# Kernel tuning notes

Measured on AMD Instinct MI355X. Metric: run time of the kernel, lower is better.

## Reference

```python
import jax, jax.numpy as jnp
import numpy as np

N_NODES = 100000
N_EDGES = 1200000
IN_DIM, HID_DIM, OUT_DIM = 64, 64, 32


def setup_inputs() -> dict:
    key = jax.random.key(0)
    k1, k2, k3, k4, k5, k6 = jax.random.split(key, 6)
    x = jax.random.normal(k1, (N_NODES, IN_DIM), dtype=jnp.float32)
    edge_index = jax.random.randint(k2, (2, N_EDGES), 0, N_NODES, dtype=jnp.int64)
    # Glorot-style init for GCN linear weights
    W1 = jax.random.normal(k3, (IN_DIM, HID_DIM), dtype=jnp.float32) / np.sqrt(IN_DIM)
    b1 = jnp.zeros((HID_DIM,), dtype=jnp.float32)
    W2 = jax.random.normal(k4, (HID_DIM, OUT_DIM), dtype=jnp.float32) / np.sqrt(HID_DIM)
    b2 = jnp.zeros((OUT_DIM,), dtype=jnp.float32)
    return {"x": x, "edge_index": edge_index, "W1": W1, "b1": b1, "W2": W2, "b2": b2}


def _gcn_conv(x, W, b, src, dst, norm, n_nodes):
    # linear transform first (PyG GCNConv): [N, out]
    h = x @ W
    # gather messages along edges (incl. self-loops), scale by sym norm
    msg = h[src] * norm[:, None]            # [E+N, out]
    out = jax.ops.segment_sum(msg, dst, num_segments=n_nodes)
    return out + b


def reference(x, edge_index, W1, b1, W2, b2):
    n_nodes = x.shape[0]
    # add self-loops (PyG GCNConv default)
    loop = jnp.arange(n_nodes, dtype=edge_index.dtype)
    src = jnp.concatenate([edge_index[0], loop])
    dst = jnp.concatenate([edge_index[1], loop])
    # symmetric normalization: deg^{-1/2}[src] * deg^{-1/2}[dst]
    deg = jax.ops.segment_sum(jnp.ones_like(dst, dtype=x.dtype), dst, num_segments=n_nodes)
    deg_isqrt = jax.lax.rsqrt(deg)          # deg >= 1 due to self-loops
    norm = deg_isqrt[src] * deg_isqrt[dst]
    h = _gcn_conv(x, W1, b1, src, dst, norm, n_nodes)
    h = jax.nn.relu(h)
    out = _gcn_conv(h, W2, b2, src, dst, norm, n_nodes)
    return out
```

## Files before the change

### kernel.cpp

```cpp
#include <hip/hip_runtime.h>
#include <hip/hip_fp16.h>
#include <type_traits>

#define NBUCK 512

typedef _Float16 half8 __attribute__((ext_vector_type(8)));
typedef float floatx4 __attribute__((ext_vector_type(4)));

__device__ inline void unpack8(const float4& raw, float* f) {
    const __half2* p = (const __half2*)&raw;
#pragma unroll
    for (int i = 0; i < 4; ++i) {
        float2 t = __half22float2(p[i]);
        f[2 * i] = t.x;
        f[2 * i + 1] = t.y;
    }
}


__global__ void bucket_hist_kernel(const int* __restrict__ dst, int* __restrict__ bucketCnt,
                                   int E, int R) {
    __shared__ int h[NBUCK];
    int tid = threadIdx.x;
    for (int i = tid; i < NBUCK; i += blockDim.x) h[i] = 0;
    __syncthreads();
    for (int i = blockIdx.x * blockDim.x + tid; i < E; i += gridDim.x * blockDim.x)
        atomicAdd(&h[dst[i] / R], 1);
    __syncthreads();
    for (int i = tid; i < NBUCK; i += blockDim.x)
        if (h[i]) atomicAdd(&bucketCnt[i], h[i]);
}


__global__ void bucket_scan_kernel(const int* __restrict__ bucketCnt, int* __restrict__ bucketBase,
                                   int* __restrict__ bucketCursor) {
    __shared__ int lds[NBUCK];
    int tid = threadIdx.x;
    int v = bucketCnt[tid];
    lds[tid] = v;
    __syncthreads();
    for (int off = 1; off < NBUCK; off <<= 1) {
        int x = (tid >= off) ? lds[tid - off] : 0;
        __syncthreads();
        lds[tid] += x;
        __syncthreads();
    }
    int excl = lds[tid] - v;
    bucketBase[tid] = excl;
    bucketCursor[tid] = excl;
    if (tid == NBUCK - 1) bucketBase[NBUCK] = lds[tid];
}


__global__ __launch_bounds__(1024) void partition_kernel(const int* __restrict__ src,
                                                         const int* __restrict__ dst,
                                                         int* __restrict__ bucketCursor,
                                                         unsigned long long* __restrict__ pairs,
                                                         int E, int R) {
    __shared__ int h[NBUCK];
    __shared__ int base[NBUCK];
    __shared__ int lcur[NBUCK];
    const int CH = 16384;
    int start = blockIdx.x * CH;
    int count = E - start;
    if (count > CH) count = CH;
    int tid = threadIdx.x;
    if (tid < NBUCK) h[tid] = 0;
    __syncthreads();
    for (int i = tid; i < count; i += 1024)
        atomicAdd(&h[dst[start + i] / R], 1);
    __syncthreads();
    if (tid < NBUCK) {
        base[tid] = h[tid] ? atomicAdd(&bucketCursor[tid], h[tid]) : 0;
        lcur[tid] = 0;
    }
    __syncthreads();
    for (int i = tid; i < count; i += 1024) {
        int d = dst[start + i];
        int s = src[start + i];
        int b = d / R;
        int r = atomicAdd(&lcur[b], 1);
        pairs[base[b] + r] = ((unsigned long long)(unsigned)s << 32) | (unsigned)d;
    }
}


__global__ void bucket_csr_kernel(const unsigned long long* __restrict__ pairs,
                                  const int* __restrict__ bucketBase, int* __restrict__ counts,
                                  int* __restrict__ offs, float* __restrict__ dinv,
                                  int* __restrict__ ssrc, int N, int R) {
    __shared__ int h[256];
    __shared__ int loffs[256];
    __shared__ int cur[256];
    int b = blockIdx.x, tid = threadIdx.x;
    int nodeBase = b * R;
    int beg = bucketBase[b], end = bucketBase[b + 1];
    h[tid] = 0;
    __syncthreads();
    for (int i = beg + tid; i < end; i += 256) {
        int d = (int)(pairs[i] & 0xffffffffull);
        atomicAdd(&h[d - nodeBase], 1);
    }
    __syncthreads();
    int v = h[tid];
    loffs[tid] = v;
    __syncthreads();
    for (int off = 1; off < 256; off <<= 1) {
        int x = (tid >= off) ? loffs[tid - off] : 0;
        __syncthreads();
        loffs[tid] += x;
        __syncthreads();
    }
    int excl = loffs[tid] - v;
    cur[tid] = excl;
    int node = nodeBase + tid;
    if (tid < R && node < N) {
        counts[node] = v;
        offs[node] = beg + excl;
        dinv[node] = rsqrtf((float)v + 1.0f);
    }
    __syncthreads();
    for (int i = beg + tid; i < end; i += 256) {
        unsigned long long p = pairs[i];
        int d = (int)(p & 0xffffffffull);
        int s = (int)(p >> 32);
        int r = atomicAdd(&cur[d - nodeBase], 1);
        ssrc[beg + r] = s;
    }
}


template <int OUTD, typename TIN>
__global__ void gemm_mfma_kernel(const TIN* __restrict__ X, const float* __restrict__ W,
                                 __half* __restrict__ H, int M, int ntiles) {
    constexpr int NC = OUTD / 16;
    const int lane = threadIdx.x & 63;
    const int wid  = threadIdx.x >> 6;
    const int q    = lane >> 4;
    const int m    = lane & 15;

    half8 bfrag[2][NC];
#pragma unroll
    for (int s = 0; s < 2; ++s)
#pragma unroll
        for (int c = 0; c < NC; ++c)
#pragma unroll
            for (int j = 0; j < 8; ++j)
                bfrag[s][c][j] = (_Float16)W[(s * 32 + q * 8 + j) * OUTD + c * 16 + m];

    for (int tile = blockIdx.x * 4 + wid; tile < ntiles; tile += gridDim.x * 4) {
        int rowBase = tile * 16;
        int rowA = rowBase + m;
        if (rowA > M - 1) rowA = M - 1;

        half8 afrag[2];
        if constexpr (std::is_same<TIN, float>::value) {
            const float4* Xr = (const float4*)(X + (size_t)rowA * 64);
#pragma unroll
            for (int s = 0; s < 2; ++s) {
                float4 v0 = Xr[s * 8 + q * 2 + 0];
                float4 v1 = Xr[s * 8 + q * 2 + 1];
                afrag[s][0] = (_Float16)v0.x;
                afrag[s][1] = (_Float16)v0.y;
                afrag[s][2] = (_Float16)v0.z;
                afrag[s][3] = (_Float16)v0.w;
                afrag[s][4] = (_Float16)v1.x;
                afrag[s][5] = (_Float16)v1.y;
                afrag[s][6] = (_Float16)v1.z;
                afrag[s][7] = (_Float16)v1.w;
            }
        } else {
            const half8* Xr = (const half8*)(X + (size_t)rowA * 64);
#pragma unroll
            for (int s = 0; s < 2; ++s)
                afrag[s] = Xr[s * 4 + q];
        }

        floatx4 acc[NC];
#pragma unroll
        for (int c = 0; c < NC; ++c) acc[c] = (floatx4){0.f, 0.f, 0.f, 0.f};
#pragma unroll
        for (int s = 0; s < 2; ++s)
#pragma unroll
            for (int c = 0; c < NC; ++c)
                acc[c] = __builtin_amdgcn_mfma_f32_16x16x32_f16(afrag[s], bfrag[s][c], acc[c],
                                                                0, 0, 0);

#pragma unroll
        for (int r = 0; r < 4; ++r) {
            int row = rowBase + q * 4 + r;
            if (row < M) {
#pragma unroll
                for (int c = 0; c < NC; ++c)
                    H[(size_t)row * OUTD + c * 16 + m] = __float2half(acc[c][r]);
            }
        }
    }
}


__global__ __launch_bounds__(256) void agg64_kernel(
    const float4* __restrict__ hrow4, const int* __restrict__ ssrc,
    const int* __restrict__ offs, const int* __restrict__ counts,
    const float* __restrict__ dinv, const float* __restrict__ b1,
    float4* __restrict__ out4, int N) {
    int tid  = threadIdx.x;
    int lane = tid & 63;
    int l    = tid & 7;
    int gb   = lane & 56;
    int node = blockIdx.x * 32 + (tid >> 3);
    if (node >= N) return;
    int beg = offs[node], cnt = counts[node];
    float a[8];
#pragma unroll
    for (int j = 0; j < 8; ++j) a[j] = 0.f;
    for (int base = 0; base < cnt; base += 8) {
        int p = base + l;
        int idx = 0;
        float dv = 0.0f;
        if (p < cnt) {
            idx = ssrc[beg + p];
            dv  = dinv[idx];
        }
#pragma unroll
        for (int j = 0; j < 8; ++j) {
            int   s  = __shfl(idx, gb | j, 64);
            float nv = __shfl(dv, gb | j, 64);
            float4 raw = hrow4[(size_t)s * 8 + l];
            float f[8];
            unpack8(raw, f);
#pragma unroll
            for (int d = 0; d < 8; ++d) a[d] = fmaf(f[d], nv, a[d]);
        }
    }
    float dd = dinv[node];
    float4 sraw = hrow4[(size_t)node * 8 + l];
    float sf[8];
    unpack8(sraw, sf);
    __half2 pk[4];
#pragma unroll
    for (int i = 0; i < 4; ++i) {
        float rx = fmaxf(dd * (a[2 * i] + sf[2 * i] * dd) + b1[8 * l + 2 * i], 0.0f);
        float ry = fmaxf(dd * (a[2 * i + 1] + sf[2 * i + 1] * dd) + b1[8 * l + 2 * i + 1], 0.0f);
        pk[i] = __floats2half2_rn(rx, ry);
    }
    out4[(size_t)node * 8 + l] = *(const float4*)pk;
}


__global__ __launch_bounds__(256) void agg32_kernel(
    const float4* __restrict__ hrow4, const int* __restrict__ ssrc,
    const int* __restrict__ offs, const int* __restrict__ counts,
    const float* __restrict__ dinv, const float* __restrict__ b2,
    float4* __restrict__ out4, int N) {
    int tid  = threadIdx.x;
    int lane = tid & 63;
    int l    = tid & 3;
    int gb   = lane & 60;
    int node = blockIdx.x * 64 + (tid >> 2);
    if (node >= N) return;
    int beg = offs[node], cnt = counts[node];
    float a[8];
#pragma unroll
    for (int j = 0; j < 8; ++j) a[j] = 0.f;
    for (int base = 0; base < cnt; base += 4) {
        int p = base + l;
        int idx = 0;
        float dv = 0.0f;
        if (p < cnt) {
            idx = ssrc[beg + p];
            dv  = dinv[idx];
        }
#pragma unroll
        for (int j = 0; j < 4; ++j) {
            int   s  = __shfl(idx, gb | j, 64);
            float nv = __shfl(dv, gb | j, 64);
            float4 raw = hrow4[(size_t)s * 4 + l];
            float f[8];
            unpack8(raw, f);
#pragma unroll
            for (int d = 0; d < 8; ++d) a[d] = fmaf(f[d], nv, a[d]);
        }
    }
    float dd = dinv[node];
    float4 sraw = hrow4[(size_t)node * 4 + l];
    float sf[8];
    unpack8(sraw, sf);
    float r[8];
#pragma unroll
    for (int j = 0; j < 8; ++j)
        r[j] = dd * (a[j] + sf[j] * dd) + b2[8 * l + j];
    out4[(size_t)node * 8 + 2 * l + 0] = make_float4(r[0], r[1], r[2], r[3]);
    out4[(size_t)node * 8 + 2 * l + 1] = make_float4(r[4], r[5], r[6], r[7]);
}


extern "C" void kernel_launch(void* const* d_in, const int* in_sizes, int n_in,
                              void* d_out, int out_size, void* d_ws, size_t ws_size,
                              hipStream_t stream) {
    const float* x  = (const float*)d_in[0];
    const int*   ei = (const int*)d_in[1];
    const float* W1 = (const float*)d_in[2];
    const float* b1 = (const float*)d_in[3];
    const float* W2 = (const float*)d_in[4];
    const float* b2 = (const float*)d_in[5];
    float* out = (float*)d_out;

    const int N = in_sizes[0] / 64;
    const int E = in_sizes[1] / 2;
    const int* src = ei;
    const int* dst = ei + E;

    const int Npad = (N + 1023) & ~1023;
    const int R    = (N + NBUCK - 1) / NBUCK;

    unsigned long long* pairs = (unsigned long long*)d_ws;
    int*   ssrc   = (int*)(pairs + E);
    int*   counts = ssrc + E;
    int*   offs   = counts + Npad;
    float* dinv   = (float*)(offs + Npad);
    int*   bucketCnt    = (int*)(dinv + Npad);
    int*   bucketBase   = bucketCnt + NBUCK;
    int*   bucketCursor = bucketBase + NBUCK + 1;
    size_t hoff = (size_t)(bucketCursor + NBUCK + 1 - (int*)d_ws);
    hoff = (hoff + 3) & ~(size_t)3;
    __half* h    = (__half*)((int*)d_ws + hoff);
    __half* out1 = h + (size_t)N * 64;
    __half* h2   = h;

    const int T = 256;

    hipMemsetAsync(bucketCnt, 0, NBUCK * sizeof(int), stream);
    bucket_hist_kernel<<<512, T, 0, stream>>>(dst, bucketCnt, E, R);
    bucket_scan_kernel<<<1, NBUCK, 0, stream>>>(bucketCnt, bucketBase, bucketCursor);
    partition_kernel<<<(E + 16383) / 16384, 1024, 0, stream>>>(src, dst, bucketCursor, pairs, E, R);
    bucket_csr_kernel<<<NBUCK, T, 0, stream>>>(pairs, bucketBase, counts, offs, dinv, ssrc, N, R);

    const int ntiles = (N + 15) / 16;

    gemm_mfma_kernel<64, float><<<782, T, 0, stream>>>(x, W1, h, N, ntiles);
    agg64_kernel<<<(N + 31) / 32, T, 0, stream>>>((const float4*)h, ssrc, offs, counts, dinv, b1,
                                                  (float4*)out1, N);

    gemm_mfma_kernel<32, __half><<<782, T, 0, stream>>>(out1, W2, h2, N, ntiles);
    agg32_kernel<<<(N + 63) / 64, T, 0, stream>>>((const float4*)h2, ssrc, offs, counts, dinv, b2,
                                                  (float4*)out, N);
}
```

Measured before the change: 220.1 us.

## Fuse histogram with first GEMM and use deterministic per-block scatter offsets

```diff
diff --git a/kernel.cpp b/kernel.cpp
--- a/kernel.cpp
+++ b/kernel.cpp
@@ -3,6 +3,7 @@
 #include <type_traits>
 
 #define NBUCK 512
+#define CH    2048
 
 typedef _Float16 half8 __attribute__((ext_vector_type(8)));
 typedef float floatx4 __attribute__((ext_vector_type(4)));
@@ -18,88 +19,165 @@
 }
 
 
-__global__ void bucket_hist_kernel(const int* __restrict__ dst, int* __restrict__ bucketCnt,
-                                   int E, int R) {
-    __shared__ int h[NBUCK];
-    int tid = threadIdx.x;
-    for (int i = tid; i < NBUCK; i += blockDim.x) h[i] = 0;
-    __syncthreads();
-    for (int i = blockIdx.x * blockDim.x + tid; i < E; i += gridDim.x * blockDim.x)
-        atomicAdd(&h[dst[i] / R], 1);
-    __syncthreads();
-    for (int i = tid; i < NBUCK; i += blockDim.x)
-        if (h[i]) atomicAdd(&bucketCnt[i], h[i]);
-}
-
-
-__global__ void bucket_scan_kernel(const int* __restrict__ bucketCnt, int* __restrict__ bucketBase,
-                                   int* __restrict__ bucketCursor) {
+__device__ inline void gemm64_f32_body(const float* __restrict__ X, const float* __restrict__ W,
+                                       __half* __restrict__ H, int M, int ntiles, int vblk,
+                                       int GB) {
+    constexpr int NC = 4;
+    const int lane = threadIdx.x & 63;
+    const int wid  = threadIdx.x >> 6;
+    const int q    = lane >> 4;
+    const int m    = lane & 15;
+
+    half8 bfrag[2][NC];
+#pragma unroll
+    for (int s = 0; s < 2; ++s)
+#pragma unroll
+        for (int c = 0; c < NC; ++c)
+#pragma unroll
+            for (int j = 0; j < 8; ++j)
+                bfrag[s][c][j] = (_Float16)W[(s * 32 + q * 8 + j) * 64 + c * 16 + m];
+
+    for (int tile = vblk * 4 + wid; tile < ntiles; tile += GB * 4) {
+        int rowBase = tile * 16;
+        int rowA = rowBase + m;
+        if (rowA > M - 1) rowA = M - 1;
+
+        half8 afrag[2];
+        const float4* Xr = (const float4*)(X + (size_t)rowA * 64);
+#pragma unroll
+        for (int s = 0; s < 2; ++s) {
+            float4 v0 = Xr[s * 8 + q * 2 + 0];
+            float4 v1 = Xr[s * 8 + q * 2 + 1];
+            afrag[s][0] = (_Float16)v0.x;
+            afrag[s][1] = (_Float16)v0.y;
+            afrag[s][2] = (_Float16)v0.z;
+            afrag[s][3] = (_Float16)v0.w;
+            afrag[s][4] = (_Float16)v1.x;
+            afrag[s][5] = (_Float16)v1.y;
+            afrag[s][6] = (_Float16)v1.z;
+            afrag[s][7] = (_Float16)v1.w;
+        }
+
+        floatx4 acc[NC];
+#pragma unroll
+        for (int c = 0; c < NC; ++c) acc[c] = (floatx4){0.f, 0.f, 0.f, 0.f};
+#pragma unroll
+        for (int s = 0; s < 2; ++s)
+#pragma unroll
+            for (int c = 0; c < NC; ++c)
+                acc[c] = __builtin_amdgcn_mfma_f32_16x16x32_f16(afrag[s], bfrag[s][c], acc[c],
+                                                                0, 0, 0);
+
+#pragma unroll
+        for (int r = 0; r < 4; ++r) {
+            int row = rowBase + q * 4 + r;
+            if (row < M) {
+#pragma unroll
+                for (int c = 0; c < NC; ++c)
+                    H[(size_t)row * 64 + c * 16 + m] = __float2half(acc[c][r]);
+            }
+        }
+    }
+}
+
+
+__global__ __launch_bounds__(256) void hist_gemm1_kernel(
+    const int* __restrict__ dst, int* __restrict__ blockHist,
+    const float* __restrict__ X, const float* __restrict__ W1, __half* __restrict__ H,
+    int M, int ntiles, int E, int R, int HB, int GB) {
+    int blk = blockIdx.x;
+    if (blk < HB) {
+        __shared__ int h[NBUCK];
+        int tid = threadIdx.x;
+        for (int i = tid; i < NBUCK; i += 256) h[i] = 0;
+        __syncthreads();
+        int start = blk * CH;
+        int count = E - start;
+        if (count > CH) count = CH;
+        for (int i = tid; i < count; i += 256) atomicAdd(&h[dst[start + i] / R], 1);
+        __syncthreads();
+        for (int i = tid; i < NBUCK; i += 256) blockHist[(size_t)blk * NBUCK + i] = h[i];
+    } else {
+        gemm64_f32_body(X, W1, H, M, ntiles, blk - HB, GB);
+    }
+}
+
+
+__global__ __launch_bounds__(NBUCK) void scan_bases_kernel(const int* __restrict__ blockHist,
+                                                           int* __restrict__ baseTbl,
+                                                           int* __restrict__ bucketStart, int HB) {
     __shared__ int lds[NBUCK];
-    int tid = threadIdx.x;
-    int v = bucketCnt[tid];
-    lds[tid] = v;
+    int b = threadIdx.x;
+    int running = 0;
+    int k = 0;
+    for (; k + 8 <= HB; k += 8) {
+        int v[8];
+#pragma unroll
+        for (int u = 0; u < 8; ++u) v[u] = blockHist[(size_t)(k + u) * NBUCK + b];
+#pragma unroll
+        for (int u = 0; u < 8; ++u) {
+            baseTbl[(size_t)(k + u) * NBUCK + b] = running;
+            running += v[u];
+        }
+    }
+    for (; k < HB; ++k) {
+        int v = blockHist[(size_t)k * NBUCK + b];
+        baseTbl[(size_t)k * NBUCK + b] = running;
+        running += v;
+    }
+    lds[b] = running;
     __syncthreads();
     for (int off = 1; off < NBUCK; off <<= 1) {
-        int x = (tid >= off) ? lds[tid - off] : 0;
-        __syncthreads();
-        lds[tid] += x;
-        __syncthreads();
-    }
-    int excl = lds[tid] - v;
-    bucketBase[tid] = excl;
-    bucketCursor[tid] = excl;
-    if (tid == NBUCK - 1) bucketBase[NBUCK] = lds[tid];
-}
-
-
-__global__ __launch_bounds__(1024) void partition_kernel(const int* __restrict__ src,
-                                                         const int* __restrict__ dst,
-                                                         int* __restrict__ bucketCursor,
-                                                         unsigned long long* __restrict__ pairs,
-                                                         int E, int R) {
-    __shared__ int h[NBUCK];
-    __shared__ int base[NBUCK];
+        int x = (b >= off) ? lds[b - off] : 0;
+        __syncthreads();
+        lds[b] += x;
+        __syncthreads();
+    }
+    bucketStart[b] = lds[b] - running;
+    if (b == NBUCK - 1) bucketStart[NBUCK] = lds[b];
+}
+
+
+__global__ __launch_bounds__(256) void scatter_kernel(
+    const int* __restrict__ src, const int* __restrict__ dst, const int* __restrict__ baseTbl,
+    const int* __restrict__ bucketStart, unsigned long long* __restrict__ pairs, int E, int R) {
     __shared__ int lcur[NBUCK];
-    const int CH = 16384;
-    int start = blockIdx.x * CH;
+    int blk = blockIdx.x, tid = threadIdx.x;
+    for (int i = tid; i < NBUCK; i += 256)
+        lcur[i] = bucketStart[i] + baseTbl[(size_t)blk * NBUCK + i];
+    __syncthreads();
+    int start = blk * CH;
     int count = E - start;
     if (count > CH) count = CH;
-    int tid = threadIdx.x;
-    if (tid < NBUCK) h[tid] = 0;
-    __syncthreads();
-    for (int i = tid; i < count; i += 1024)
-        atomicAdd(&h[dst[start + i] / R], 1);
-    __syncthreads();
-    if (tid < NBUCK) {
-        base[tid] = h[tid] ? atomicAdd(&bucketCursor[tid], h[tid]) : 0;
-        lcur[tid] = 0;
-    }
-    __syncthreads();
-    for (int i = tid; i < count; i += 1024) {
+    for (int i = tid; i < count; i += 256) {
         int d = dst[start + i];
         int s = src[start + i];
         int b = d / R;
         int r = atomicAdd(&lcur[b], 1);
-        pairs[base[b] + r] = ((unsigned long long)(unsigned)s << 32) | (unsigned)d;
-    }
-}
-
-
-__global__ void bucket_csr_kernel(const unsigned long long* __restrict__ pairs,
-                                  const int* __restrict__ bucketBase, int* __restrict__ counts,
-                                  int* __restrict__ offs, float* __restrict__ dinv,
-                                  int* __restrict__ ssrc, int N, int R) {
+        pairs[r] = ((unsigned long long)(unsigned)s << 32) | (unsigned)d;
+    }
+}
+
+
+__global__ __launch_bounds__(256) void bucket_csr_kernel(
+    const unsigned long long* __restrict__ pairs, const int* __restrict__ bucketStart,
+    int* __restrict__ counts, int* __restrict__ offs, float* __restrict__ dinv,
+    int* __restrict__ ssrc, int N, int R) {
+    __shared__ unsigned long long stage[3072];
     __shared__ int h[256];
     __shared__ int loffs[256];
     __shared__ int cur[256];
     int b = blockIdx.x, tid = threadIdx.x;
     int nodeBase = b * R;
-    int beg = bucketBase[b], end = bucketBase[b + 1];
+    int beg = bucketStart[b], end = bucketStart[b + 1];
+    int len = end - beg;
+    int sl = len < 3072 ? len : 3072;
+    for (int i = tid; i < sl; i += 256) stage[i] = pairs[beg + i];
     h[tid] = 0;
     __syncthreads();
-    for (int i = beg + tid; i < end; i += 256) {
-        int d = (int)(pairs[i] & 0xffffffffull);
-        atomicAdd(&h[d - nodeBase], 1);
+    for (int i = tid; i < len; i += 256) {
+        unsigned long long p = (i < 3072) ? stage[i] : pairs[beg + i];
+        atomicAdd(&h[(int)(p & 0xffffffffull) - nodeBase], 1);
     }
     __syncthreads();
     int v = h[tid];
@@ -120,20 +198,21 @@
         dinv[node] = rsqrtf((float)v + 1.0f);
     }
     __syncthreads();
-    for (int i = beg + tid; i < end; i += 256) {
-        unsigned long long p = pairs[i];
-        int d = (int)(p & 0xffffffffull);
+    for (int i = tid; i < len; i += 256) {
+        unsigned long long p = (i < 3072) ? stage[i] : pairs[beg + i];
+        int d = (int)(p & 0xffffffffull) - nodeBase;
         int s = (int)(p >> 32);
-        int r = atomicAdd(&cur[d - nodeBase], 1);
+        int r = atomicAdd(&cur[d], 1);
         ssrc[beg + r] = s;
     }
 }
 
 
-template <int OUTD, typename TIN>
-__global__ void gemm_mfma_kernel(const TIN* __restrict__ X, const float* __restrict__ W,
-                                 __half* __restrict__ H, int M, int ntiles) {
-    constexpr int NC = OUTD / 16;
+__global__ __launch_bounds__(256) void gemm2_mfma_kernel(const __half* __restrict__ X,
+                                                         const float* __restrict__ W,
+                                                         __half* __restrict__ H, int M,
+                                                         int ntiles) {
+    constexpr int NC = 2;
     const int lane = threadIdx.x & 63;
     const int wid  = threadIdx.x >> 6;
     const int q    = lane >> 4;
@@ -146,35 +225,17 @@
         for (int c = 0; c < NC; ++c)
 #pragma unroll
             for (int j = 0; j < 8; ++j)
-                bfrag[s][c][j] = (_Float16)W[(s * 32 + q * 8 + j) * OUTD + c * 16 + m];
+                bfrag[s][c][j] = (_Float16)W[(s * 32 + q * 8 + j) * 32 + c * 16 + m];
 
     for (int tile = blockIdx.x * 4 + wid; tile < ntiles; tile += gridDim.x * 4) {
         int rowBase = tile * 16;
         int rowA = rowBase + m;
         if (rowA > M - 1) rowA = M - 1;
 
+        const half8* Xr = (const half8*)(X + (size_t)rowA * 64);
         half8 afrag[2];
-        if constexpr (std::is_same<TIN, float>::value) {
-            const float4* Xr = (const float4*)(X + (size_t)rowA * 64);
-#pragma unroll
-            for (int s = 0; s < 2; ++s) {
-                float4 v0 = Xr[s * 8 + q * 2 + 0];
-                float4 v1 = Xr[s * 8 + q * 2 + 1];
-                afrag[s][0] = (_Float16)v0.x;
-                afrag[s][1] = (_Float16)v0.y;
-                afrag[s][2] = (_Float16)v0.z;
-                afrag[s][3] = (_Float16)v0.w;
-                afrag[s][4] = (_Float16)v1.x;
-                afrag[s][5] = (_Float16)v1.y;
-                afrag[s][6] = (_Float16)v1.z;
-                afrag[s][7] = (_Float16)v1.w;
-            }
-        } else {
-            const half8* Xr = (const half8*)(X + (size_t)rowA * 64);
-#pragma unroll
-            for (int s = 0; s < 2; ++s)
-                afrag[s] = Xr[s * 4 + q];
-        }
+#pragma unroll
+        for (int s = 0; s < 2; ++s) afrag[s] = Xr[s * 4 + q];
 
         floatx4 acc[NC];
 #pragma unroll
@@ -192,7 +253,7 @@
             if (row < M) {
 #pragma unroll
                 for (int c = 0; c < NC; ++c)
-                    H[(size_t)row * OUTD + c * 16 + m] = __float2half(acc[c][r]);
+                    H[(size_t)row * 32 + c * 16 + m] = __float2half(acc[c][r]);
             }
         }
     }
@@ -313,36 +374,34 @@
 
     const int Npad = (N + 1023) & ~1023;
     const int R    = (N + NBUCK - 1) / NBUCK;
+    const int HB   = (E + CH - 1) / CH;
+    const int GB   = 782;
 
     unsigned long long* pairs = (unsigned long long*)d_ws;
-    int*   ssrc   = (int*)(pairs + E);
-    int*   counts = ssrc + E;
-    int*   offs   = counts + Npad;
-    float* dinv   = (float*)(offs + Npad);
-    int*   bucketCnt    = (int*)(dinv + Npad);
-    int*   bucketBase   = bucketCnt + NBUCK;
-    int*   bucketCursor = bucketBase + NBUCK + 1;
-    size_t hoff = (size_t)(bucketCursor + NBUCK + 1 - (int*)d_ws);
+    int*   ssrc        = (int*)(pairs + E);
+    int*   counts      = ssrc + E;
+    int*   offs        = counts + Npad;
+    float* dinv        = (float*)(offs + Npad);
+    int*   bucketStart = (int*)(dinv + Npad);
+    int*   blockHist   = bucketStart + NBUCK + 2;
+    int*   baseTbl     = blockHist + (size_t)HB * NBUCK;
+    size_t hoff = (size_t)(baseTbl + (size_t)HB * NBUCK - (int*)d_ws);
     hoff = (hoff + 3) & ~(size_t)3;
     __half* h    = (__half*)((int*)d_ws + hoff);
     __half* out1 = h + (size_t)N * 64;
     __half* h2   = h;
 
-    const int T = 256;
-
-    hipMemsetAsync(bucketCnt, 0, NBUCK * sizeof(int), stream);
-    bucket_hist_kernel<<<512, T, 0, stream>>>(dst, bucketCnt, E, R);
-    bucket_scan_kernel<<<1, NBUCK, 0, stream>>>(bucketCnt, bucketBase, bucketCursor);
-    partition_kernel<<<(E + 16383) / 16384, 1024, 0, stream>>>(src, dst, bucketCursor, pairs, E, R);
-    bucket_csr_kernel<<<NBUCK, T, 0, stream>>>(pairs, bucketBase, counts, offs, dinv, ssrc, N, R);
-
     const int ntiles = (N + 15) / 16;
 
-    gemm_mfma_kernel<64, float><<<782, T, 0, stream>>>(x, W1, h, N, ntiles);
-    agg64_kernel<<<(N + 31) / 32, T, 0, stream>>>((const float4*)h, ssrc, offs, counts, dinv, b1,
-                                                  (float4*)out1, N);
-
-    gemm_mfma_kernel<32, __half><<<782, T, 0, stream>>>(out1, W2, h2, N, ntiles);
-    agg32_kernel<<<(N + 63) / 64, T, 0, stream>>>((const float4*)h2, ssrc, offs, counts, dinv, b2,
-                                                  (float4*)out, N);
-}
+    hist_gemm1_kernel<<<HB + GB, 256, 0, stream>>>(dst, blockHist, x, W1, h, N, ntiles,
+                                                   E, R, HB, GB);
+    scan_bases_kernel<<<1, NBUCK, 0, stream>>>(blockHist, baseTbl, bucketStart, HB);
+    scatter_kernel<<<HB, 256, 0, stream>>>(src, dst, baseTbl, bucketStart, pairs, E, R);
+    bucket_csr_kernel<<<NBUCK, 256, 0, stream>>>(pairs, bucketStart, counts, offs, dinv, ssrc,
+                                                 N, R);
+    agg64_kernel<<<(N + 31) / 32, 256, 0, stream>>>((const float4*)h, ssrc, offs, counts, dinv,
+                                                    b1, (float4*)out1, N);
+    gemm2_mfma_kernel<<<782, 256, 0, stream>>>(out1, W2, h2, N, ntiles);
+    agg32_kernel<<<(N + 63) / 64, 256, 0, stream>>>((const float4*)h2, ssrc, offs, counts, dinv,
+                                                    b2, (float4*)out, N);
+}
```

Result: slower. 227.3 us (+3.3%).

## Fuse histogram with layer-1 GEMM, use fixed-capacity buckets, fold W2 GEMV into aggregation

Applied to the files above, without the earlier changes.

```diff
diff --git a/kernel.cpp b/kernel.cpp
--- a/kernel.cpp
+++ b/kernel.cpp
@@ -1,8 +1,10 @@
 #include <hip/hip_runtime.h>
 #include <hip/hip_fp16.h>
-#include <type_traits>
 
 #define NBUCK 512
+#define CH    4096
+#define CAP   4096
+#define VTOT  1024
 
 typedef _Float16 half8 __attribute__((ext_vector_type(8)));
 typedef float floatx4 __attribute__((ext_vector_type(4)));
@@ -18,97 +20,130 @@
 }
 
 
-__global__ void bucket_hist_kernel(const int* __restrict__ dst, int* __restrict__ bucketCnt,
-                                   int E, int R) {
-    __shared__ int h[NBUCK];
-    int tid = threadIdx.x;
-    for (int i = tid; i < NBUCK; i += blockDim.x) h[i] = 0;
-    __syncthreads();
-    for (int i = blockIdx.x * blockDim.x + tid; i < E; i += gridDim.x * blockDim.x)
-        atomicAdd(&h[dst[i] / R], 1);
-    __syncthreads();
-    for (int i = tid; i < NBUCK; i += blockDim.x)
-        if (h[i]) atomicAdd(&bucketCnt[i], h[i]);
-}
-
-
-__global__ void bucket_scan_kernel(const int* __restrict__ bucketCnt, int* __restrict__ bucketBase,
-                                   int* __restrict__ bucketCursor) {
-    __shared__ int lds[NBUCK];
-    int tid = threadIdx.x;
-    int v = bucketCnt[tid];
-    lds[tid] = v;
-    __syncthreads();
-    for (int off = 1; off < NBUCK; off <<= 1) {
-        int x = (tid >= off) ? lds[tid - off] : 0;
+__global__ __launch_bounds__(256) void k_phaseA(
+    const int* __restrict__ dst, int* __restrict__ baseTbl, int* __restrict__ cursor,
+    const float* __restrict__ X, const float* __restrict__ W1, __half* __restrict__ H,
+    int M, int ntiles, int E, int R, int HB) {
+    int blk = blockIdx.x;
+    if (blk < HB) {
+        __shared__ int h[NBUCK];
+        int tid = threadIdx.x;
+        for (int i = tid; i < NBUCK; i += 256) h[i] = 0;
         __syncthreads();
-        lds[tid] += x;
+        int start = blk * CH;
+        int count = E - start;
+        if (count > CH) count = CH;
+        for (int i = tid; i < count; i += 256) atomicAdd(&h[dst[start + i] / R], 1);
         __syncthreads();
-    }
-    int excl = lds[tid] - v;
-    bucketBase[tid] = excl;
-    bucketCursor[tid] = excl;
-    if (tid == NBUCK - 1) bucketBase[NBUCK] = lds[tid];
-}
-
-
-__global__ __launch_bounds__(1024) void partition_kernel(const int* __restrict__ src,
-                                                         const int* __restrict__ dst,
-                                                         int* __restrict__ bucketCursor,
-                                                         unsigned long long* __restrict__ pairs,
-                                                         int E, int R) {
-    __shared__ int h[NBUCK];
-    __shared__ int base[NBUCK];
+        for (int i = tid; i < NBUCK; i += 256) {
+            int c = h[i];
+            int base = c ? atomicAdd(&cursor[i], c) : 0;
+            baseTbl[(size_t)blk * NBUCK + i] = base;
+        }
+    } else {
+        const int GB = VTOT - HB;
+        const int vblk = blk - HB;
+        const int lane = threadIdx.x & 63;
+        const int wid  = threadIdx.x >> 6;
+        const int q    = lane >> 4;
+        const int m    = lane & 15;
+
+        half8 bfrag[2][4];
+#pragma unroll
+        for (int s = 0; s < 2; ++s)
+#pragma unroll
+            for (int c = 0; c < 4; ++c)
+#pragma unroll
+                for (int j = 0; j < 8; ++j)
+                    bfrag[s][c][j] = (_Float16)W1[(s * 32 + q * 8 + j) * 64 + c * 16 + m];
+
+        for (int tile = vblk * 4 + wid; tile < ntiles; tile += GB * 4) {
+            int rowBase = tile * 16;
+            int rowA = rowBase + m;
+            if (rowA > M - 1) rowA = M - 1;
+            const float4* Xr = (const float4*)(X + (size_t)rowA * 64);
+            half8 afrag[2];
+#pragma unroll
+            for (int s = 0; s < 2; ++s) {
+                float4 v0 = Xr[s * 8 + q * 2 + 0];
+                float4 v1 = Xr[s * 8 + q * 2 + 1];
+                afrag[s][0] = (_Float16)v0.x; afrag[s][1] = (_Float16)v0.y;
+                afrag[s][2] = (_Float16)v0.z; afrag[s][3] = (_Float16)v0.w;
+                afrag[s][4] = (_Float16)v1.x; afrag[s][5] = (_Float16)v1.y;
+                afrag[s][6] = (_Float16)v1.z; afrag[s][7] = (_Float16)v1.w;
+            }
+            floatx4 acc[4];
+#pragma unroll
+            for (int c = 0; c < 4; ++c) acc[c] = (floatx4){0.f, 0.f, 0.f, 0.f};
+#pragma unroll
+            for (int s = 0; s < 2; ++s)
+#pragma unroll
+                for (int c = 0; c < 4; ++c)
+                    acc[c] = __builtin_amdgcn_mfma_f32_16x16x32_f16(afrag[s], bfrag[s][c],
+                                                                    acc[c], 0, 0, 0);
+#pragma unroll
+            for (int r = 0; r < 4; ++r) {
+                int row = rowBase + q * 4 + r;
+                if (row < M) {
+#pragma unroll
+                    for (int c = 0; c < 4; ++c)
+                        H[(size_t)row * 64 + c * 16 + m] = __float2half(acc[c][r]);
+                }
+            }
+        }
+    }
+}
+
+
+__global__ __launch_bounds__(256) void k_scatter(
+    const int* __restrict__ src, const int* __restrict__ dst, const int* __restrict__ baseTbl,
+    unsigned long long* __restrict__ pairs, int E, int R) {
     __shared__ int lcur[NBUCK];
-    const int CH = 16384;
-    int start = blockIdx.x * CH;
+    int blk = blockIdx.x, tid = threadIdx.x;
+    for (int i = tid; i < NBUCK; i += 256)
+        lcur[i] = i * CAP + baseTbl[(size_t)blk * NBUCK + i];
+    __syncthreads();
+    int start = blk * CH;
     int count = E - start;
     if (count > CH) count = CH;
-    int tid = threadIdx.x;
-    if (tid < NBUCK) h[tid] = 0;
-    __syncthreads();
-    for (int i = tid; i < count; i += 1024)
-        atomicAdd(&h[dst[start + i] / R], 1);
-    __syncthreads();
-    if (tid < NBUCK) {
-        base[tid] = h[tid] ? atomicAdd(&bucketCursor[tid], h[tid]) : 0;
-        lcur[tid] = 0;
-    }
-    __syncthreads();
-    for (int i = tid; i < count; i += 1024) {
+    for (int i = tid; i < count; i += 256) {
         int d = dst[start + i];
         int s = src[start + i];
         int b = d / R;
         int r = atomicAdd(&lcur[b], 1);
-        pairs[base[b] + r] = ((unsigned long long)(unsigned)s << 32) | (unsigned)d;
-    }
-}
-
-
-__global__ void bucket_csr_kernel(const unsigned long long* __restrict__ pairs,
-                                  const int* __restrict__ bucketBase, int* __restrict__ counts,
-                                  int* __restrict__ offs, float* __restrict__ dinv,
-                                  int* __restrict__ ssrc, int N, int R) {
+        pairs[r] = ((unsigned long long)(unsigned)s << 32) | (unsigned)d;
+    }
+}
+
+
+__global__ __launch_bounds__(256) void k_csr(
+    const unsigned long long* __restrict__ pairs, const int* __restrict__ cursor,
+    int* __restrict__ counts, int* __restrict__ offs, float* __restrict__ dinv,
+    int* __restrict__ ssrc, int N, int R) {
+    __shared__ unsigned long long stage[3072];
     __shared__ int h[256];
     __shared__ int loffs[256];
     __shared__ int cur[256];
     int b = blockIdx.x, tid = threadIdx.x;
     int nodeBase = b * R;
-    int beg = bucketBase[b], end = bucketBase[b + 1];
+    int beg = b * CAP;
+    int len = cursor[b];
+    int sl = len < 3072 ? len : 3072;
+    for (int i = tid; i < sl; i += 256) stage[i] = pairs[beg + i];
     h[tid] = 0;
     __syncthreads();
-    for (int i = beg + tid; i < end; i += 256) {
-        int d = (int)(pairs[i] & 0xffffffffull);
-        atomicAdd(&h[d - nodeBase], 1);
+    for (int i = tid; i < len; i += 256) {
+        unsigned long long pr = (i < 3072) ? stage[i] : pairs[beg + i];
+        atomicAdd(&h[(int)(pr & 0xffffffffull) - nodeBase], 1);
     }
     __syncthreads();
     int v = h[tid];
     loffs[tid] = v;
     __syncthreads();
     for (int off = 1; off < 256; off <<= 1) {
-        int x = (tid >= off) ? loffs[tid - off] : 0;
+        int xv = (tid >= off) ? loffs[tid - off] : 0;
         __syncthreads();
-        loffs[tid] += x;
+        loffs[tid] += xv;
         __syncthreads();
     }
     int excl = loffs[tid] - v;
@@ -120,90 +155,21 @@
         dinv[node] = rsqrtf((float)v + 1.0f);
     }
     __syncthreads();
-    for (int i = beg + tid; i < end; i += 256) {
-        unsigned long long p = pairs[i];
-        int d = (int)(p & 0xffffffffull);
-        int s = (int)(p >> 32);
-        int r = atomicAdd(&cur[d - nodeBase], 1);
+    for (int i = tid; i < len; i += 256) {
+        unsigned long long pr = (i < 3072) ? stage[i] : pairs[beg + i];
+        int d = (int)(pr & 0xffffffffull) - nodeBase;
+        int s = (int)(pr >> 32);
+        int r = atomicAdd(&cur[d], 1);
         ssrc[beg + r] = s;
     }
 }
 
 
-template <int OUTD, typename TIN>
-__global__ void gemm_mfma_kernel(const TIN* __restrict__ X, const float* __restrict__ W,
-                                 __half* __restrict__ H, int M, int ntiles) {
-    constexpr int NC = OUTD / 16;
-    const int lane = threadIdx.x & 63;
-    const int wid  = threadIdx.x >> 6;
-    const int q    = lane >> 4;
-    const int m    = lane & 15;
-
-    half8 bfrag[2][NC];
-#pragma unroll
-    for (int s = 0; s < 2; ++s)
-#pragma unroll
-        for (int c = 0; c < NC; ++c)
-#pragma unroll
-            for (int j = 0; j < 8; ++j)
-                bfrag[s][c][j] = (_Float16)W[(s * 32 + q * 8 + j) * OUTD + c * 16 + m];
-
-    for (int tile = blockIdx.x * 4 + wid; tile < ntiles; tile += gridDim.x * 4) {
-        int rowBase = tile * 16;
-        int rowA = rowBase + m;
-        if (rowA > M - 1) rowA = M - 1;
-
-        half8 afrag[2];
-        if constexpr (std::is_same<TIN, float>::value) {
-            const float4* Xr = (const float4*)(X + (size_t)rowA * 64);
-#pragma unroll
-            for (int s = 0; s < 2; ++s) {
-                float4 v0 = Xr[s * 8 + q * 2 + 0];
-                float4 v1 = Xr[s * 8 + q * 2 + 1];
-                afrag[s][0] = (_Float16)v0.x;
-                afrag[s][1] = (_Float16)v0.y;
-                afrag[s][2] = (_Float16)v0.z;
-                afrag[s][3] = (_Float16)v0.w;
-                afrag[s][4] = (_Float16)v1.x;
-                afrag[s][5] = (_Float16)v1.y;
-                afrag[s][6] = (_Float16)v1.z;
-                afrag[s][7] = (_Float16)v1.w;
-            }
-        } else {
-            const half8* Xr = (const half8*)(X + (size_t)rowA * 64);
-#pragma unroll
-            for (int s = 0; s < 2; ++s)
-                afrag[s] = Xr[s * 4 + q];
-        }
-
-        floatx4 acc[NC];
-#pragma unroll
-        for (int c = 0; c < NC; ++c) acc[c] = (floatx4){0.f, 0.f, 0.f, 0.f};
-#pragma unroll
-        for (int s = 0; s < 2; ++s)
-#pragma unroll
-            for (int c = 0; c < NC; ++c)
-                acc[c] = __builtin_amdgcn_mfma_f32_16x16x32_f16(afrag[s], bfrag[s][c], acc[c],
-                                                                0, 0, 0);
-
-#pragma unroll
-        for (int r = 0; r < 4; ++r) {
-            int row = rowBase + q * 4 + r;
-            if (row < M) {
-#pragma unroll
-                for (int c = 0; c < NC; ++c)
-                    H[(size_t)row * OUTD + c * 16 + m] = __float2half(acc[c][r]);
-            }
-        }
-    }
-}
-
-
-__global__ __launch_bounds__(256) void agg64_kernel(
+__global__ __launch_bounds__(256) void k_agg64gemv(
     const float4* __restrict__ hrow4, const int* __restrict__ ssrc,
     const int* __restrict__ offs, const int* __restrict__ counts,
     const float* __restrict__ dinv, const float* __restrict__ b1,
-    float4* __restrict__ out4, int N) {
+    const float* __restrict__ W2, __half* __restrict__ h2, int N) {
     int tid  = threadIdx.x;
     int lane = tid & 63;
     int l    = tid & 7;
@@ -215,11 +181,11 @@
 #pragma unroll
     for (int j = 0; j < 8; ++j) a[j] = 0.f;
     for (int base = 0; base < cnt; base += 8) {
-        int p = base + l;
+        int pos = base + l;
         int idx = 0;
         float dv = 0.0f;
-        if (p < cnt) {
-            idx = ssrc[beg + p];
+        if (pos < cnt) {
+            idx = ssrc[beg + pos];
             dv  = dinv[idx];
         }
 #pragma unroll
@@ -237,18 +203,34 @@
     float4 sraw = hrow4[(size_t)node * 8 + l];
     float sf[8];
     unpack8(sraw, sf);
-    __half2 pk[4];
-#pragma unroll
-    for (int i = 0; i < 4; ++i) {
-        float rx = fmaxf(dd * (a[2 * i] + sf[2 * i] * dd) + b1[8 * l + 2 * i], 0.0f);
-        float ry = fmaxf(dd * (a[2 * i + 1] + sf[2 * i + 1] * dd) + b1[8 * l + 2 * i + 1], 0.0f);
-        pk[i] = __floats2half2_rn(rx, ry);
-    }
-    out4[(size_t)node * 8 + l] = *(const float4*)pk;
-}
-
-
-__global__ __launch_bounds__(256) void agg32_kernel(
+    float r[8];
+#pragma unroll
+    for (int j = 0; j < 8; ++j)
+        r[j] = fmaxf(dd * (a[j] + sf[j] * dd) + b1[8 * l + j], 0.0f);
+
+    float acc0 = 0.f, acc1 = 0.f, acc2 = 0.f, acc3 = 0.f;
+#pragma unroll
+    for (int slp = 0; slp < 8; ++slp) {
+#pragma unroll
+        for (int ddp = 0; ddp < 8; ++ddp) {
+            float v = __shfl(r[ddp], gb | slp, 64);
+            float4 w = *(const float4*)(W2 + (slp * 8 + ddp) * 32 + 4 * l);
+            acc0 = fmaf(v, w.x, acc0);
+            acc1 = fmaf(v, w.y, acc1);
+            acc2 = fmaf(v, w.z, acc2);
+            acc3 = fmaf(v, w.w, acc3);
+        }
+    }
+    __half2 o01 = __floats2half2_rn(acc0, acc1);
+    __half2 o23 = __floats2half2_rn(acc2, acc3);
+    float2 pack;
+    pack.x = *(const float*)&o01;
+    pack.y = *(const float*)&o23;
+    *(float2*)(h2 + (size_t)node * 32 + 4 * l) = pack;
+}
+
+
+__global__ __launch_bounds__(256) void k_agg32(
     const float4* __restrict__ hrow4, const int* __restrict__ ssrc,
     const int* __restrict__ offs, const int* __restrict__ counts,
     const float* __restrict__ dinv, const float* __restrict__ b2,
@@ -264,11 +246,11 @@
 #pragma unroll
     for (int j = 0; j < 8; ++j) a[j] = 0.f;
     for (int base = 0; base < cnt; base += 4) {
-        int p = base + l;
+        int pos = base + l;
         int idx = 0;
         float dv = 0.0f;
-        if (p < cnt) {
-            idx = ssrc[beg + p];
+        if (pos < cnt) {
+            idx = ssrc[beg + pos];
             dv  = dinv[idx];
         }
 #pragma unroll
@@ -304,7 +286,6 @@
     const float* b1 = (const float*)d_in[3];
     const float* W2 = (const float*)d_in[4];
     const float* b2 = (const float*)d_in[5];
-    float* out = (float*)d_out;
 
     const int N = in_sizes[0] / 64;
     const int E = in_sizes[1] / 2;
@@ -313,36 +294,28 @@
 
     const int Npad = (N + 1023) & ~1023;
     const int R    = (N + NBUCK - 1) / NBUCK;
-
-    unsigned long long* pairs = (unsigned long long*)d_ws;
-    int*   ssrc   = (int*)(pairs + E);
-    int*   counts = ssrc + E;
-    int*   offs   = counts + Npad;
-    float* dinv   = (float*)(offs + Npad);
-    int*   bucketCnt    = (int*)(dinv + Npad);
-    int*   bucketBase   = bucketCnt + NBUCK;
-    int*   bucketCursor = bucketBase + NBUCK + 1;
-    size_t hoff = (size_t)(bucketCursor + NBUCK + 1 - (int*)d_ws);
-    hoff = (hoff + 3) & ~(size_t)3;
-    __half* h    = (__half*)((int*)d_ws + hoff);
-    __half* out1 = h + (size_t)N * 64;
-    __half* h2   = h;
-
-    const int T = 256;
-
-    hipMemsetAsync(bucketCnt, 0, NBUCK * sizeof(int), stream);
-    bucket_hist_kernel<<<512, T, 0, stream>>>(dst, bucketCnt, E, R);
-    bucket_scan_kernel<<<1, NBUCK, 0, stream>>>(bucketCnt, bucketBase, bucketCursor);
-    partition_kernel<<<(E + 16383) / 16384, 1024, 0, stream>>>(src, dst, bucketCursor, pairs, E, R);
-    bucket_csr_kernel<<<NBUCK, T, 0, stream>>>(pairs, bucketBase, counts, offs, dinv, ssrc, N, R);
+    const int HB   = (E + CH - 1) / CH;
+
+    char* w = (char*)d_ws;
+    unsigned long long* pairs = (unsigned long long*)w;  w += (size_t)NBUCK * CAP * 8;
+    int*   ssrc    = (int*)w;                            w += (size_t)NBUCK * CAP * 4;
+    int*   counts  = (int*)w;                            w += (size_t)Npad * 4;
+    int*   offs    = (int*)w;                            w += (size_t)Npad * 4;
+    float* dinv    = (float*)w;                          w += (size_t)Npad * 4;
+    int*   baseTbl = (int*)w;                            w += (size_t)HB * NBUCK * 4;
+    int*   cursor  = (int*)w;                            w += (size_t)(NBUCK + 4) * 4;
+    __half* h  = (__half*)w;                             w += (size_t)N * 64 * 2;
+    __half* h2 = (__half*)w;                             w += (size_t)N * 32 * 2;
 
     const int ntiles = (N + 15) / 16;
 
-    gemm_mfma_kernel<64, float><<<782, T, 0, stream>>>(x, W1, h, N, ntiles);
-    agg64_kernel<<<(N + 31) / 32, T, 0, stream>>>((const float4*)h, ssrc, offs, counts, dinv, b1,
-                                                  (float4*)out1, N);
-
-    gemm_mfma_kernel<32, __half><<<782, T, 0, stream>>>(out1, W2, h2, N, ntiles);
-    agg32_kernel<<<(N + 63) / 64, T, 0, stream>>>((const float4*)h2, ssrc, offs, counts, dinv, b2,
-                                                  (float4*)out, N);
-}
+    hipMemsetAsync(cursor, 0, NBUCK * sizeof(int), stream);
+
+    k_phaseA<<<VTOT, 256, 0, stream>>>(dst, baseTbl, cursor, x, W1, h, N, ntiles, E, R, HB);
+    k_scatter<<<HB, 256, 0, stream>>>(src, dst, baseTbl, pairs, E, R);
+    k_csr<<<NBUCK, 256, 0, stream>>>(pairs, cursor, counts, offs, dinv, ssrc, N, R);
+    k_agg64gemv<<<(N + 31) / 32, 256, 0, stream>>>((const float4*)h, ssrc, offs, counts, dinv,
+                                                   b1, W2, h2, N);
+    k_agg32<<<(N + 63) / 64, 256, 0, stream>>>((const float4*)h2, ssrc, offs, counts, dinv, b2,
+                                               (float4*)d_out, N);
+}
```

Measured after the change: 196.6 us. 1.12x faster.
